# Kernel optimization log

Measured on AMD Instinct MI355X. Metric: run time of the kernel, lower is better.

The kernel has to match this reference:

```python
import jax, jax.numpy as jnp
import numpy as np
from jax import lax

DN = ('NCHW', 'OIHW', 'NCHW')

def conv(x, w, b, stride=1, pad=0):
    y = lax.conv_general_dilated(x, w, (stride, stride), ((pad, pad), (pad, pad)), dimension_numbers=DN)
    return y + b[None, :, None, None]

def conv_transpose(x, w, b):
    # torch ConvTranspose2d(k=4, s=2, p=1): w is (in_ch, out_ch, 4, 4)
    wf = jnp.flip(w, (2, 3)).transpose(1, 0, 2, 3)  # -> (out_ch, in_ch, 4, 4)
    pad = 4 - 1 - 1  # k - 1 - p = 2
    y = lax.conv_general_dilated(x, wf, (1, 1), ((pad, pad), (pad, pad)), lhs_dilation=(2, 2), dimension_numbers=DN)
    return y + b[None, :, None, None]

def setup_inputs() -> dict:
    key = jax.random.key(0)
    ks = jax.random.split(key, 16)
    HID, ZC, K = 256, 64, 512
    def w(k, shape):
        return (jax.random.normal(k, shape, jnp.float32) * 0.02)
    z = lambda n: jnp.zeros((n,), jnp.float32)
    return {
        'x': jax.random.uniform(ks[0], (8, 3, 128, 128), jnp.float32),
        'c1_w': w(ks[1], (HID, 3, 4, 4)), 'c1_b': z(HID),
        'c2_w': w(ks[2], (HID, HID, 4, 4)), 'c2_b': z(HID),
        'r0_w3': w(ks[3], (HID, HID, 3, 3)), 'r0_b3': z(HID),
        'r0_w1': w(ks[4], (HID, HID, 1, 1)), 'r0_b1': z(HID),
        'r1_w3': w(ks[5], (HID, HID, 3, 3)), 'r1_b3': z(HID),
        'r1_w1': w(ks[6], (HID, HID, 1, 1)), 'r1_b1': z(HID),
        'to_z_w': w(ks[7], (ZC, HID, 1, 1)), 'to_z_b': z(ZC),
        'codebook': jax.random.uniform(ks[8], (K, ZC), jnp.float32, -1.0 / K, 1.0 / K),
        'from_z_w': w(ks[9], (HID, ZC, 1, 1)), 'from_z_b': z(HID),
        't1_w': w(ks[10], (HID, HID, 4, 4)), 't1_b': z(HID),
        't2_w': w(ks[11], (HID, 3, 4, 4)), 't2_b': z(3),
    }

def _vqvae(x, c1_w, c1_b, c2_w, c2_b, r0_w3, r0_b3, r0_w1, r0_b1,
           r1_w3, r1_b3, r1_w1, r1_b1, to_z_w, to_z_b, codebook,
           from_z_w, from_z_b, t1_w, t1_b, t2_w, t2_b):
    # ---- Encoder ----
    h = jax.nn.relu(conv(x, c1_w, c1_b, stride=2, pad=1))
    h = jax.nn.relu(conv(h, c2_w, c2_b, stride=2, pad=1))
    for (w3, b3, w1, b1) in ((r0_w3, r0_b3, r0_w1, r0_b1), (r1_w3, r1_b3, r1_w1, r1_b1)):
        r = conv(jax.nn.relu(h), w3, b3, pad=1)
        r = conv(jax.nn.relu(r), w1, b1)
        h = h + r
    z_e = conv(h, to_z_w, to_z_b)  # [B, ZC, H/4, W/4]
    # ---- Vector quantization ----
    B, C, H, W = z_e.shape
    z_flat = z_e.transpose(0, 2, 3, 1).reshape(-1, C)  # [N, C]
    dist = (jnp.sum(z_flat * z_flat, axis=1, keepdims=True)
            - 2.0 * z_flat @ codebook.T
            + jnp.sum(codebook * codebook, axis=1)[None, :])  # [N, K]
    ids = jnp.argmin(dist, axis=1)  # [N]
    e_k_flat = codebook[ids]  # [N, C]
    e_k_st_flat = z_flat + lax.stop_gradient(e_k_flat - z_flat)
    e_k = e_k_flat.reshape(B, H, W, C).transpose(0, 3, 1, 2)
    e_k_st = e_k_st_flat.reshape(B, H, W, C).transpose(0, 3, 1, 2)
    ids = ids.reshape(B, H, W)
    # ---- Decoder ----
    d = jax.nn.relu(conv(e_k_st, from_z_w, from_z_b))
    d = jax.nn.relu(conv_transpose(d, t1_w, t1_b))
    out = jax.nn.sigmoid(conv_transpose(d, t2_w, t2_b))
    return out, z_e, e_k, ids

def reference(x, c1_w, c1_b, c2_w, c2_b, r0_w3, r0_b3, r0_w1, r0_b1,
              r1_w3, r1_b3, r1_w1, r1_b1, to_z_w, to_z_b, codebook,
              from_z_w, from_z_b, t1_w, t1_b, t2_w, t2_b):
    return _vqvae(x, c1_w, c1_b, c2_w, c2_b, r0_w3, r0_b3, r0_w1, r0_b1,
                  r1_w3, r1_b3, r1_w1, r1_b1, to_z_w, to_z_b, codebook,
                  from_z_w, from_z_b, t1_w, t1_b, t2_w, t2_b)
```

## Files before the change

### kernel.cpp

```cpp
#include <hip/hip_runtime.h>
#include <math.h>


typedef unsigned int uint;
typedef unsigned short ushort_t;
using short8 = __attribute__((ext_vector_type(8))) short;
using f32x4  = __attribute__((ext_vector_type(4))) float;

__device__ __attribute__((aligned(16))) ushort_t g_zpad[512];

static __device__ __forceinline__ int rfl(int x) { return __builtin_amdgcn_readfirstlane(x); }
static __device__ __forceinline__ ushort_t f2bf(float f) {
  uint u = __float_as_uint(f);
  return (ushort_t)((u + 0x7fffu + ((u >> 16) & 1u)) >> 16);
}
static __device__ __forceinline__ float bf2f(ushort_t b) {
  return __uint_as_float(((uint)b) << 16);
}
static __device__ __forceinline__ void gload16(const ushort_t* g, void* l) {
  __builtin_amdgcn_global_load_lds(
      (const __attribute__((address_space(1))) void*)g,
      (__attribute__((address_space(3))) void*)l, 16, 0, 0);
}

__global__ __launch_bounds__(256) void k_prep_misc(
    const float* __restrict__ c1w, float* __restrict__ wt_c1,
    const float* __restrict__ tozw, float* __restrict__ wt_toz,
    const float* __restrict__ fromzw, float* __restrict__ wt_fromz,
    const float* __restrict__ cb, float* __restrict__ cnorm,
    const float* __restrict__ t2w, ushort_t* __restrict__ w2pk)
{
  const int b = blockIdx.x, tid = threadIdx.x;
  if (b < 48) {
    int idx = b * 256 + tid;
    int co = idx % 256, i = idx / 256;
    wt_c1[idx] = c1w[co * 48 + i];
  } else if (b < 112) {
    int idx = (b - 48) * 256 + tid;
    int co = idx % 64, i = idx / 64;
    wt_toz[idx] = tozw[co * 256 + i];
  } else if (b < 176) {
    int idx = (b - 112) * 256 + tid;
    int co = idx % 256, i = idx / 256;
    wt_fromz[idx] = fromzw[co * 64 + i];
  } else if (b < 178) {
    int idx = (b - 176) * 256 + tid;
    if (idx < 512) {
      float s = 0.f;
      for (int c = 0; c < 64; ++c) { float v = cb[idx * 64 + c]; s = fmaf(v, v, s); }
      cnorm[idx] = s;
    }
  } else {
    int idx = (b - 178) * 256 + tid;
    int k = idx & 31, co = (idx >> 5) & 15, chunk = (idx >> 9) & 31, par = idx >> 14;
    int tap = chunk >> 3, cg = chunk & 7;
    int a = tap >> 1, bb = tap & 1;
    int ry = par & 1, rx = (par >> 1) & 1;
    int ky = ((ry + 1) & 1) + 2 * a;
    int kx = ((rx + 1) & 1) + 2 * bb;
    int ci = cg * 32 + k;
    float v = (co < 3) ? t2w[((ci * 3 + co) << 4) + ky * 4 + kx] : 0.f;
    w2pk[idx] = f2bf(v);
  }
}

template<int KIND>
__global__ __launch_bounds__(256) void k_prep_enc(
    const float* __restrict__ w, ushort_t* __restrict__ wp)
{
  constexpr int KK = (KIND == 0) ? 16 : (KIND == 1 ? 9 : 1);
  constexpr int KW = (KIND == 0) ? 4  : (KIND == 1 ? 3 : 1);
  constexpr int NT = KK;
  const int tid = threadIdx.x;
  const int wvg = blockIdx.x * 4 + (tid >> 6);
  const int lane = tid & 63;
  const int co = wvg >> 2;
  const int ci = (wvg & 3) * 64 + lane;
  const float* src = w + (size_t)(co * 256 + ci) * KK;
  const int coT = co >> 6, row = co & 63, cg = ci >> 5, k = ci & 31;
  float v[KK];
#pragma unroll
  for (int j = 0; j < KK; ++j) v[j] = src[j];
#pragma unroll
  for (int tap = 0; tap < NT; ++tap) {
    int ky, kx;
    if (KIND == 0)      { ky = tap >> 2; kx = tap & 3; }
    else if (KIND == 1) { ky = tap / 3;  kx = tap - ky * 3; }
    else                { ky = 0; kx = 0; }
    float val = v[ky * KW + kx];
    ushort_t b0 = f2bf(val);
    ushort_t b1 = f2bf(val - bf2f(b0));
    const int chunk = tap * 8 + cg;
    size_t base = ((size_t)(chunk * 4 + coT) << 12) + row * 32 + k;
    wp[base] = b0;
    wp[base + 2048] = b1;
  }
}

template<int KIND>
__global__ __launch_bounds__(256) void k_prep_enc2(
    const float* __restrict__ wa, ushort_t* __restrict__ oa,
    const float* __restrict__ wb2, ushort_t* __restrict__ ob)
{
  constexpr int KK = (KIND == 0) ? 16 : (KIND == 1 ? 9 : 1);
  constexpr int KW = (KIND == 0) ? 4  : (KIND == 1 ? 3 : 1);
  constexpr int NT = KK;
  const float* w = (blockIdx.x < 256) ? wa : wb2;
  ushort_t* wp = (blockIdx.x < 256) ? oa : ob;
  const int bx = blockIdx.x & 255;
  const int tid = threadIdx.x;
  const int wvg = bx * 4 + (tid >> 6);
  const int lane = tid & 63;
  const int co = wvg >> 2;
  const int ci = (wvg & 3) * 64 + lane;
  const float* src = w + (size_t)(co * 256 + ci) * KK;
  const int coT = co >> 6, row = co & 63, cg = ci >> 5, k = ci & 31;
  float v[KK];
#pragma unroll
  for (int j = 0; j < KK; ++j) v[j] = src[j];
#pragma unroll
  for (int tap = 0; tap < NT; ++tap) {
    int ky, kx;
    if (KIND == 0)      { ky = tap >> 2; kx = tap & 3; }
    else if (KIND == 1) { ky = tap / 3;  kx = tap - ky * 3; }
    else                { ky = 0; kx = 0; }
    float val = v[ky * KW + kx];
    ushort_t b0 = f2bf(val);
    ushort_t b1 = f2bf(val - bf2f(b0));
    const int chunk = tap * 8 + cg;
    size_t base = ((size_t)(chunk * 4 + coT) << 12) + row * 32 + k;
    wp[base] = b0;
    wp[base + 2048] = b1;
  }
}

__global__ void k_prep_t1w(const float* __restrict__ w, ushort_t* __restrict__ wb) {
  int idx = blockIdx.x * 256 + threadIdx.x;
  int kk  = idx & 31;
  int co  = (idx >> 5) & 255;
  int c8  = (idx >> 13) & 7;
  int tap = (idx >> 16) & 3;
  int par = idx >> 18;
  int ry = par & 1, rx = (par >> 1) & 1;
  int a = tap >> 1, b = tap & 1;
  int ky = ((ry + 1) & 1) + 2 * a;
  int kx = ((rx + 1) & 1) + 2 * b;
  int ci = c8 * 32 + kk;
  wb[idx] = f2bf(w[((ci * 256 + co) << 4) + ky * 4 + kx]);
}

__global__ __launch_bounds__(256) void k_conv1_split(
    const float* __restrict__ in, ushort_t* __restrict__ o0, ushort_t* __restrict__ o1,
    const float* __restrict__ wT, const float* __restrict__ bias)
{
  __shared__ float s_in[3 * 360];
  const int tid = threadIdx.x;
  const int lane = tid & 63;
  const int wv = rfl(tid >> 6);
  const int px = lane & 7, py = lane >> 3;
  const int tx = blockIdx.x & 7, ty = blockIdx.x >> 3;
  const int X = tx * 8, Y = ty * 8;
  const int cob = blockIdx.y * 64 + wv * 16;
  const int n = blockIdx.z;
  float acc[16];
#pragma unroll
  for (int i = 0; i < 16; ++i) acc[i] = bias[cob + i];
  const float* inN = in + (size_t)n * 3 * 16384;
  for (int e = tid; e < 3 * 360; e += 256) {
    int col2 = e % 20; int t = e / 20; int row = t % 18; int ci = t / 18;
    int pr = col2 / 10, hc = col2 % 10, ixl = 2 * hc + pr;
    int iy = 2 * Y - 1 + row, ix = 2 * X - 1 + ixl;
    float v = 0.f;
    if (ixl < 18 && (unsigned)iy < 128u && (unsigned)ix < 128u)
      v = inN[ci * 16384 + iy * 128 + ix];
    s_in[e] = v;
  }
  __syncthreads();
  const float* wc = wT + cob;
#pragma unroll
  for (int c = 0; c < 3; ++c) {
    const float* base = s_in + c * 360 + py * 40 + px;
#pragma unroll
    for (int ky = 0; ky < 4; ++ky) {
#pragma unroll
      for (int kx = 0; kx < 4; ++kx) {
        float iv = base[ky * 20 + (kx & 1) * 10 + (kx >> 1)];
        const float* w = wc + (size_t)(c * 16 + ky * 4 + kx) * 256;
#pragma unroll
        for (int i = 0; i < 16; ++i) acc[i] = fmaf(iv, w[i], acc[i]);
      }
    }
  }
  const int pxg = n * 4096 + (Y + py) * 64 + (X + px);
  uint p0[8], p1[8];
#pragma unroll
  for (int i = 0; i < 8; ++i) {
    float va = fmaxf(acc[2 * i], 0.f), vb = fmaxf(acc[2 * i + 1], 0.f);
    ushort_t a0 = f2bf(va), b0 = f2bf(vb);
    ushort_t a1 = f2bf(va - bf2f(a0)), b1 = f2bf(vb - bf2f(b0));
    p0[i] = (uint)a0 | ((uint)b0 << 16);
    p1[i] = (uint)a1 | ((uint)b1 << 16);
  }
  ushort_t* d0 = o0 + (size_t)pxg * 256 + cob;
  ushort_t* d1 = o1 + (size_t)pxg * 256 + cob;
  uint4 v0a; v0a.x = p0[0]; v0a.y = p0[1]; v0a.z = p0[2]; v0a.w = p0[3];
  uint4 v0b; v0b.x = p0[4]; v0b.y = p0[5]; v0b.z = p0[6]; v0b.w = p0[7];
  uint4 v1a; v1a.x = p1[0]; v1a.y = p1[1]; v1a.z = p1[2]; v1a.w = p1[3];
  uint4 v1b; v1b.x = p1[4]; v1b.y = p1[5]; v1b.z = p1[6]; v1b.w = p1[7];
  *(uint4*)d0 = v0a; *(uint4*)(d0 + 8) = v0b;
  *(uint4*)d1 = v1a; *(uint4*)(d1 + 8) = v1b;
}

template<int KIND>
__global__ __launch_bounds__(256) void k_enc_mfma_split(
    const ushort_t* __restrict__ x0, const ushort_t* __restrict__ x1,
    const ushort_t* __restrict__ wp, float* __restrict__ part)
{
  __shared__ ushort_t smem[2][12288];
  const int tid = threadIdx.x, lane = tid & 63, wv = tid >> 6;
  const int l15 = lane & 15, q = lane >> 4;
  const int pxT = blockIdx.x, coT = blockIdx.y;
  constexpr int NCH = (KIND == 0) ? 128 : 72;
  const int CH0 = blockIdx.z * (NCH / 2), CH1 = CH0 + NCH / 2;
  f32x4 acc[4][2];
#pragma unroll
  for (int m = 0; m < 4; ++m)
#pragma unroll
    for (int n = 0; n < 2; ++n) acc[m][n] = (f32x4){0.f, 0.f, 0.f, 0.f};

  const int r0 = tid >> 2, kq = tid & 3;
  int bimg[2], bu[2], bvc[2];
#pragma unroll
  for (int r = 0; r < 2; ++r) {
    int bpx = pxT * 128 + r0 + r * 64;
    bimg[r] = bpx >> 10; int bp = bpx & 1023; bu[r] = bp >> 5; bvc[r] = bp & 31;
  }
  const ushort_t* srcB[2][2];
  int ptap = -1;
  auto retap = [&](int tap) {
    ptap = tap;
    int ky, kx;
    if (KIND == 0) { ky = tap >> 2; kx = tap & 3; }
    else           { ky = tap / 3;  kx = tap - ky * 3; }
#pragma unroll
    for (int r = 0; r < 2; ++r) {
      bool v; size_t rowb;
      if (KIND == 0) {
        int iy = 2 * bu[r] - 1 + ky, ix = 2 * bvc[r] - 1 + kx;
        v = ((unsigned)iy < 64u) && ((unsigned)ix < 64u);
        rowb = ((size_t)(bimg[r] * 4096 + iy * 64 + ix)) << 8;
      } else {
        int iy = bu[r] - 1 + ky, ix = bvc[r] - 1 + kx;
        v = ((unsigned)iy < 32u) && ((unsigned)ix < 32u);
        rowb = ((size_t)(bimg[r] * 1024 + iy * 32 + ix)) << 8;
      }
      srcB[r][0] = (v ? (x0 + rowb) : g_zpad) + kq * 8;
      srcB[r][1] = (v ? (x1 + rowb) : g_zpad) + kq * 8;
    }
  };

  const int wvb = wv * 1024;
  auto stage = [&](int chunk, int bi) {
    const int tap = chunk >> 3, cg = chunk & 7;
    if (tap != ptap) retap(tap);
    char* bufb = (char*)smem[bi];
    const ushort_t* ap = wp + ((size_t)(chunk * 4 + coT) << 12) + tid * 8;
    gload16(ap,        bufb + wvb);
    gload16(ap + 2048, bufb + 4096 + wvb);
    const int ko = cg * 32;
    gload16(srcB[0][0] + ko, bufb + 8192 + wvb);
    gload16(srcB[1][0] + ko, bufb + 8192 + 4096 + wvb);
    gload16(srcB[0][1] + ko, bufb + 16384 + wvb);
    gload16(srcB[1][1] + ko, bufb + 16384 + 4096 + wvb);
  };
  auto compute = [&](const ushort_t* buf) {
    const ushort_t* sA = buf;
    const ushort_t* sB = buf + 4096;
    short8 af[4][2], bf[2][2];
#pragma unroll
    for (int m = 0; m < 4; ++m)
#pragma unroll
      for (int pl = 0; pl < 2; ++pl)
        af[m][pl] = *(const short8*)(sA + pl * 2048 + (m * 16 + l15) * 32 + q * 8);
#pragma unroll
    for (int n = 0; n < 2; ++n)
#pragma unroll
      for (int pl = 0; pl < 2; ++pl)
        bf[n][pl] = *(const short8*)(sB + pl * 4096 + (wv * 32 + n * 16 + l15) * 32 + q * 8);
#pragma unroll
    for (int m = 0; m < 4; ++m)
#pragma unroll
      for (int n = 0; n < 2; ++n) {
        acc[m][n] = __builtin_amdgcn_mfma_f32_16x16x32_bf16(af[m][0], bf[n][0], acc[m][n], 0, 0, 0);
        acc[m][n] = __builtin_amdgcn_mfma_f32_16x16x32_bf16(af[m][0], bf[n][1], acc[m][n], 0, 0, 0);
        acc[m][n] = __builtin_amdgcn_mfma_f32_16x16x32_bf16(af[m][1], bf[n][0], acc[m][n], 0, 0, 0);
      }
  };

  stage(CH0, 0);
  __syncthreads();
  int cur = 0;
  for (int c = CH0; c < CH1; ++c) {
    if (c + 1 < CH1) stage(c + 1, cur ^ 1);
    compute(smem[cur]);
    __syncthreads();
    cur ^= 1;
  }

  float* pz = part + ((size_t)blockIdx.z << 21);
#pragma unroll
  for (int m = 0; m < 4; ++m) {
#pragma unroll
    for (int n = 0; n < 2; ++n) {
#pragma unroll
      for (int r = 0; r < 4; ++r) {
        const int co_l = m * 16 + q * 4 + r;
        const int px_l = wv * 32 + n * 16 + l15;
        const int px = pxT * 128 + px_l;
        const int img = px >> 10, pp = px & 1023;
        const size_t ha = ((size_t)(img * 256 + coT * 64 + co_l)) * 1024 + pp;
        pz[ha] = acc[m][n][r];
      }
    }
  }
}

__global__ __launch_bounds__(256) void k_enc_mfma_3x3h(
    const ushort_t* __restrict__ x0, const ushort_t* __restrict__ x1,
    const ushort_t* __restrict__ wp, float* __restrict__ part)
{
  __shared__ ushort_t smem[32768];
  const int tid = threadIdx.x, lane = tid & 63, wv = tid >> 6;
  const int l15 = lane & 15, q = lane >> 4;
  const int pxT = blockIdx.x, coT = blockIdx.y;
  const int CG0 = blockIdx.z * 4;
  const int img = pxT >> 3;
  const int U0 = (pxT & 7) * 4;
  f32x4 acc[2][2];
#pragma unroll
  for (int m = 0; m < 2; ++m)
#pragma unroll
    for (int n = 0; n < 2; ++n) acc[m][n] = (f32x4){0.f, 0.f, 0.f, 0.f};

  const ushort_t* srcp[7];
#pragma unroll
  for (int i = 0; i < 7; ++i) {
    int slot = i * 256 + tid;
    int pl = slot >= 816 ? 1 : 0;
    int rem = slot - pl * 816;
    int rr = rem / 136;
    int c4 = rem - rr * 136;
    int cc = c4 >> 2, kq2 = c4 & 3;
    int iy = U0 - 1 + rr, ix = cc - 1;
    bool valid = (slot < 1632) && ((unsigned)iy < 32u) && ((unsigned)ix < 32u);
    const ushort_t* base = valid
        ? ((pl ? x1 : x0) + (((size_t)(img * 1024 + iy * 32 + ix)) << 8))
        : g_zpad;
    srcp[i] = base + kq2 * 8;
  }
  const int apl = tid >> 7;
  const int aus = apl * 2048 + (coT & 1) * 1024 + (tid & 127) * 8;
  const int coTq = coT >> 1;
  const int wvb = wv * 1024;
  char* bufb = (char*)smem;

  for (int cg = CG0; cg < CG0 + 4; ++cg) {
#pragma unroll
    for (int tap = 0; tap < 9; ++tap) {
      const int chunk = tap * 8 + cg;
      gload16(wp + ((size_t)(chunk * 4 + coTq) << 12) + aus, bufb + tap * 4096 + wvb);
    }
    const int ko = cg * 32;
#pragma unroll
    for (int i = 0; i < 7; ++i)
      gload16(srcp[i] + ko, bufb + 36864 + i * 4096 + wvb);
    __syncthreads();
    const ushort_t* Ab = smem;
    const ushort_t* Hb = smem + 18432;
#pragma unroll 3
    for (int tap = 0; tap < 9; ++tap) {
      const int ky = tap / 3, kx = tap - ky * 3;
      short8 af[2][2], bf[2][2];
#pragma unroll
      for (int m = 0; m < 2; ++m)
#pragma unroll
        for (int pl = 0; pl < 2; ++pl)
          af[m][pl] = *(const short8*)(Ab + tap * 2048 + pl * 1024 + (m * 16 + l15) * 32 + q * 8);
      const int r = wv + ky;
#pragma unroll
      for (int n = 0; n < 2; ++n)
#pragma unroll
        for (int pl = 0; pl < 2; ++pl)
          bf[n][pl] = *(const short8*)(Hb + pl * 6528 + r * 1088 + (n * 16 + l15 + kx) * 32 + q * 8);
#pragma unroll
      for (int m = 0; m < 2; ++m)
#pragma unroll
        for (int n = 0; n < 2; ++n) {
          acc[m][n] = __builtin_amdgcn_mfma_f32_16x16x32_bf16(af[m][0], bf[n][0], acc[m][n], 0, 0, 0);
          acc[m][n] = __builtin_amdgcn_mfma_f32_16x16x32_bf16(af[m][0], bf[n][1], acc[m][n], 0, 0, 0);
          acc[m][n] = __builtin_amdgcn_mfma_f32_16x16x32_bf16(af[m][1], bf[n][0], acc[m][n], 0, 0, 0);
        }
    }
    __syncthreads();
  }

  float* pz = part + ((size_t)blockIdx.z << 21);
#pragma unroll
  for (int m = 0; m < 2; ++m) {
#pragma unroll
    for (int n = 0; n < 2; ++n) {
#pragma unroll
      for (int r = 0; r < 4; ++r) {
        const int co_l = m * 16 + q * 4 + r;
        const int px_l = wv * 32 + n * 16 + l15;
        const int px = pxT * 128 + px_l;
        const int imgp = px >> 10, pp = px & 1023;
        const size_t ha = ((size_t)(imgp * 256 + coT * 32 + co_l)) * 1024 + pp;
        pz[ha] = acc[m][n][r];
      }
    }
  }
}

template<bool WH>
__global__ __launch_bounds__(256) void k_enc_epi(
    const float* __restrict__ part, float* __restrict__ h32,
    ushort_t* __restrict__ s0, ushort_t* __restrict__ s1,
    const float* __restrict__ bias)
{
  const int px = blockIdx.x * 256 + threadIdx.x;
  const int co0 = blockIdx.y * 16;
  const int img = px >> 10, pp = px & 1023;
  const float* part1 = part + (1u << 21);
  uint p0[8], p1[8];
#pragma unroll
  for (int i = 0; i < 8; ++i) {
    size_t ha = ((size_t)(img * 256 + co0 + 2 * i)) * 1024 + pp;
    size_t hb = ha + 1024;
    float va = part[ha] + part1[ha] + bias[co0 + 2 * i];
    float vb = part[hb] + part1[hb] + bias[co0 + 2 * i + 1];
    float sa, sb;
    if (WH) {
      va = fmaxf(va, 0.f); vb = fmaxf(vb, 0.f);
      h32[ha] = va; h32[hb] = vb; sa = va; sb = vb;
    } else { sa = fmaxf(va, 0.f); sb = fmaxf(vb, 0.f); }
    ushort_t a0 = f2bf(sa), b0 = f2bf(sb);
    p0[i] = (uint)a0 | ((uint)b0 << 16);
    p1[i] = (uint)f2bf(sa - bf2f(a0)) | ((uint)f2bf(sb - bf2f(b0)) << 16);
  }
  ushort_t* d0 = s0 + (size_t)px * 256 + co0;
  ushort_t* d1 = s1 + (size_t)px * 256 + co0;
  uint4 v0a; v0a.x = p0[0]; v0a.y = p0[1]; v0a.z = p0[2]; v0a.w = p0[3];
  uint4 v0b; v0b.x = p0[4]; v0b.y = p0[5]; v0b.z = p0[6]; v0b.w = p0[7];
  uint4 v1a; v1a.x = p1[0]; v1a.y = p1[1]; v1a.z = p1[2]; v1a.w = p1[3];
  uint4 v1b; v1b.x = p1[4]; v1b.y = p1[5]; v1b.z = p1[6]; v1b.w = p1[7];
  *(uint4*)d0 = v0a; *(uint4*)(d0 + 8) = v0b;
  *(uint4*)d1 = v1a; *(uint4*)(d1 + 8) = v1b;
}

template<bool WS>
__global__ __launch_bounds__(256) void k_enc_mfma(
    const ushort_t* __restrict__ x0, const ushort_t* __restrict__ x1,
    const ushort_t* __restrict__ wp, const float* __restrict__ bias,
    float* __restrict__ h32, ushort_t* __restrict__ sp0, ushort_t* __restrict__ sp1)
{
  __shared__ ushort_t smem[24576];
  const int tid = threadIdx.x, lane = tid & 63, wv = tid >> 6;
  const int l15 = lane & 15, q = lane >> 4;
  const int pxT = blockIdx.x, coT = blockIdx.y;
  f32x4 acc[4][2];
#pragma unroll
  for (int m = 0; m < 4; ++m)
#pragma unroll
    for (int n = 0; n < 2; ++n) acc[m][n] = (f32x4){0.f, 0.f, 0.f, 0.f};

  const int r0 = tid >> 2, kq = tid & 3;
  const ushort_t* srcB[2][2];
#pragma unroll
  for (int r = 0; r < 2; ++r) {
    size_t rowb = ((size_t)(pxT * 128 + r0 + r * 64)) << 8;
    srcB[r][0] = x0 + rowb + kq * 8;
    srcB[r][1] = x1 + rowb + kq * 8;
  }
  const int wvb = wv * 1024;
  auto stage = [&](int c, int bi) {
    char* bufb = (char*)(smem + bi * 12288);
    const ushort_t* ap = wp + ((size_t)(c * 4 + coT) << 12) + tid * 8;
    gload16(ap,        bufb + wvb);
    gload16(ap + 2048, bufb + 4096 + wvb);
    const int ko = c * 32;
    gload16(srcB[0][0] + ko, bufb + 8192 + wvb);
    gload16(srcB[1][0] + ko, bufb + 8192 + 4096 + wvb);
    gload16(srcB[0][1] + ko, bufb + 16384 + wvb);
    gload16(srcB[1][1] + ko, bufb + 16384 + 4096 + wvb);
  };
  auto compute = [&](const ushort_t* buf) {
    const ushort_t* sA = buf;
    const ushort_t* sB = buf + 4096;
    short8 af[4][2], bf[2][2];
#pragma unroll
    for (int m = 0; m < 4; ++m)
#pragma unroll
      for (int pl = 0; pl < 2; ++pl)
        af[m][pl] = *(const short8*)(sA + pl * 2048 + (m * 16 + l15) * 32 + q * 8);
#pragma unroll
    for (int n = 0; n < 2; ++n)
#pragma unroll
      for (int pl = 0; pl < 2; ++pl)
        bf[n][pl] = *(const short8*)(sB + pl * 4096 + (wv * 32 + n * 16 + l15) * 32 + q * 8);
#pragma unroll
    for (int m = 0; m < 4; ++m)
#pragma unroll
      for (int n = 0; n < 2; ++n) {
        acc[m][n] = __builtin_amdgcn_mfma_f32_16x16x32_bf16(af[m][0], bf[n][0], acc[m][n], 0, 0, 0);
        acc[m][n] = __builtin_amdgcn_mfma_f32_16x16x32_bf16(af[m][0], bf[n][1], acc[m][n], 0, 0, 0);
        acc[m][n] = __builtin_amdgcn_mfma_f32_16x16x32_bf16(af[m][1], bf[n][0], acc[m][n], 0, 0, 0);
      }
  };

  stage(0, 0);
  __syncthreads();
  int cur = 0;
  for (int c = 0; c < 8; ++c) {
    if (c + 1 < 8) stage(c + 1, cur ^ 1);
    compute(smem + cur * 12288);
    __syncthreads();
    cur ^= 1;
  }

#pragma unroll
  for (int m = 0; m < 4; ++m) {
#pragma unroll
    for (int n = 0; n < 2; ++n) {
#pragma unroll
      for (int r = 0; r < 4; ++r) {
        const int co_l = m * 16 + q * 4 + r;
        const int px_l = wv * 32 + n * 16 + l15;
        float v = acc[m][n][r] + bias[coT * 64 + co_l];
        const int px = pxT * 128 + px_l;
        const int img = px >> 10, pp = px & 1023;
        const size_t ha = ((size_t)(img * 256 + coT * 64 + co_l)) * 1024 + pp;
        v += h32[ha];
        h32[ha] = v;
        if (WS) {
          float sv = fmaxf(v, 0.f);
          ushort_t b0 = f2bf(sv);
          smem[px_l * 72 + co_l] = b0;
          smem[9216 + px_l * 72 + co_l] = f2bf(sv - bf2f(b0));
        }
      }
    }
  }
  if (WS) {
    __syncthreads();
#pragma unroll
    for (int i = 0; i < 8; ++i) {
      int idx = tid + 256 * i;
      int pl = idx >> 10, w2 = idx & 1023, pxl = w2 >> 3, g = w2 & 7;
      uint4 vv = *(const uint4*)(smem + pl * 9216 + pxl * 72 + g * 8);
      ushort_t* dst = (pl ? sp1 : sp0) + ((size_t)(pxT * 128 + pxl)) * 256 + coT * 64 + g * 8;
      *(uint4*)dst = vv;
    }
  }
}

__global__ __launch_bounds__(256) void k_conv1x1(
    const float* __restrict__ in, float* __restrict__ out,
    const float* __restrict__ wT, const float* __restrict__ bias,
    int CI, int CO, int P)
{
  const int p = blockIdx.x * 256 + threadIdx.x;
  const int cob = blockIdx.y * 16;
  const int n = blockIdx.z;
  const float* inN = in + (size_t)n * CI * P + p;
  float acc[16];
#pragma unroll
  for (int i = 0; i < 16; ++i) acc[i] = bias[cob + i];
  const float* wr = wT + cob;
#pragma unroll 4
  for (int ci = 0; ci < CI; ++ci) {
    float iv = inN[(size_t)ci * P];
    const float* w = wr + (size_t)ci * CO;
#pragma unroll
    for (int i = 0; i < 16; ++i) acc[i] = fmaf(iv, w[i], acc[i]);
  }
  float* outN = out + (size_t)n * CO * P + p;
#pragma unroll
  for (int i = 0; i < 16; ++i) outN[(size_t)(cob + i) * P] = acc[i];
}

__global__ __launch_bounds__(256) void k_vq_part(
    const float* __restrict__ z_e, const float* __restrict__ cb,
    const float* __restrict__ cnorm, float* __restrict__ pbest, int* __restrict__ pbid)
{
  int g = blockIdx.x * 256 + threadIdx.x;
  int chunk = blockIdx.y;
  int img = g >> 10, p = g & 1023;
  const float* zp = z_e + (size_t)img * 64 * 1024 + p;
  float z[64];
#pragma unroll
  for (int c = 0; c < 64; ++c) z[c] = zp[(size_t)c * 1024];
  float best = 3.4e38f; int bid = chunk << 5;
  const int j0 = chunk << 5;
  for (int j = j0; j < j0 + 32; ++j) {
    const float* cj = cb + j * 64;
    float m = 0.f;
#pragma unroll
    for (int c = 0; c < 64; ++c) m = fmaf(z[c], cj[c], m);
    float d = fmaf(-2.f, m, cnorm[j]);
    if (d < best) { best = d; bid = j; }
  }
  pbest[chunk * 8192 + g] = best;
  pbid[chunk * 8192 + g] = bid;
}

__global__ __launch_bounds__(256) void k_vq_reduce(
    const float* __restrict__ pbest, const int* __restrict__ pbid,
    const float* __restrict__ cb, float* __restrict__ ids_f, float* __restrict__ ek)
{
  int g = blockIdx.x * 256 + threadIdx.x;
  float best = 3.4e38f; int bid = 0;
#pragma unroll
  for (int ch = 0; ch < 16; ++ch) {
    float d = pbest[ch * 8192 + g];
    int b = pbid[ch * 8192 + g];
    if (d < best) { best = d; bid = b; }
  }
  ids_f[g] = (float)bid;
  int img = g >> 10, p = g & 1023;
  const float* cbid = cb + bid * 64;
  float* ekp = ek + (size_t)img * 64 * 1024 + p;
#pragma unroll
  for (int c = 0; c < 64; ++c) ekp[(size_t)c * 1024] = cbid[c];
}

__global__ __launch_bounds__(256) void k_from_z(
    const float* __restrict__ ek, ushort_t* __restrict__ nhwc,
    const float* __restrict__ wT, const float* __restrict__ bias)
{
  const int p = blockIdx.x * 256 + threadIdx.x;
  const int co0 = blockIdx.y * 16;
  const int n = blockIdx.z;
  const float* inN = ek + (size_t)n * 64 * 1024 + p;
  float acc[16];
#pragma unroll
  for (int i = 0; i < 16; ++i) acc[i] = bias[co0 + i];
#pragma unroll 4
  for (int ci = 0; ci < 64; ++ci) {
    float iv = inN[(size_t)ci * 1024];
    const float* w = wT + (size_t)ci * 256 + co0;
#pragma unroll
    for (int i = 0; i < 16; ++i) acc[i] = fmaf(iv, w[i], acc[i]);
  }
  uint pk[8];
#pragma unroll
  for (int i = 0; i < 8; ++i) {
    ushort_t lo = f2bf(fmaxf(acc[2 * i], 0.f));
    ushort_t hi = f2bf(fmaxf(acc[2 * i + 1], 0.f));
    pk[i] = (uint)lo | ((uint)hi << 16);
  }
  ushort_t* op = nhwc + (((size_t)n * 1024 + p) * 256 + co0);
  uint4 v0; v0.x = pk[0]; v0.y = pk[1]; v0.z = pk[2]; v0.w = pk[3];
  uint4 v1; v1.x = pk[4]; v1.y = pk[5]; v1.z = pk[6]; v1.w = pk[7];
  *(uint4*)(op) = v0;
  *(uint4*)(op + 8) = v1;
}

__global__ __launch_bounds__(256) void k_mfma_t1(
    const ushort_t* __restrict__ nhwc, const ushort_t* __restrict__ wb,
    const float* __restrict__ bias, ushort_t* __restrict__ t1o)
{
  __shared__ ushort_t smem[2][8192];
  const int tid = threadIdx.x;
  const int lane = tid & 63;
  const int wv = tid >> 6;
  const int wm = wv & 1, wn = wv >> 1;
  const int l15 = lane & 15, q = lane >> 4;
  const int pxT = blockIdx.x, coT = blockIdx.y, par = blockIdx.z;
  const int ry = par & 1, rx = (par >> 1) & 1;
  const int pxbase = pxT * 128;
  const int img = pxbase >> 10;
  f32x4 acc[4][4];
#pragma unroll
  for (int i = 0; i < 4; ++i)
#pragma unroll
    for (int j = 0; j < 4; ++j) acc[i][j] = (f32x4){0.f, 0.f, 0.f, 0.f};

  const int srow = tid >> 2, kg = tid & 3;
  int bu2[2], bv2[2];
#pragma unroll
  for (int r = 0; r < 2; ++r) {
    int px = pxbase + srow + r * 64;
    bu2[r] = (px >> 5) & 31; bv2[r] = px & 31;
  }
  const ushort_t* nb[2];
  int ptap = -1;
  auto retap = [&](int tap) {
    ptap = tap;
    int ta = tap >> 1, tb = tap & 1;
#pragma unroll
    for (int r = 0; r < 2; ++r) {
      int iy = bu2[r] + ry - ta, ix = bv2[r] + rx - tb;
      bool v = ((unsigned)iy < 32u) && ((unsigned)ix < 32u);
      nb[r] = (v ? (nhwc + (((size_t)(img * 1024 + iy * 32 + ix)) << 8)) : g_zpad) + kg * 8;
    }
  };
  const int wvb = wv * 1024;
  auto stage = [&](int c, int bi) {
    const int tap = c >> 3, c8 = c & 7;
    if (tap != ptap) retap(tap);
    char* bufb = (char*)smem[bi];
    const ushort_t* Abase = wb + ((size_t)((par * 4 + tap) * 8 + c8) << 13) + coT * 4096 + tid * 8;
    gload16(Abase,        bufb + wvb);
    gload16(Abase + 2048, bufb + 4096 + wvb);
    const int ko = c8 * 32;
    gload16(nb[0] + ko, bufb + 8192 + wvb);
    gload16(nb[1] + ko, bufb + 8192 + 4096 + wvb);
  };
  auto compute = [&](const ushort_t* buf) {
    const ushort_t* sA = buf;
    const ushort_t* sB = buf + 4096;
    short8 af[4], bfr[4];
#pragma unroll
    for (int i = 0; i < 4; ++i)
      af[i] = *(const short8*)(sA + (wm * 64 + i * 16 + l15) * 32 + q * 8);
#pragma unroll
    for (int j = 0; j < 4; ++j)
      bfr[j] = *(const short8*)(sB + (wn * 64 + j * 16 + l15) * 32 + q * 8);
#pragma unroll
    for (int i = 0; i < 4; ++i)
#pragma unroll
      for (int j = 0; j < 4; ++j)
        acc[i][j] = __builtin_amdgcn_mfma_f32_16x16x32_bf16(af[i], bfr[j], acc[i][j], 0, 0, 0);
  };

  stage(0, 0);
  __syncthreads();
  int cur = 0;
  for (int c = 0; c < 32; ++c) {
    if (c + 1 < 32) stage(c + 1, cur ^ 1);
    compute(smem[cur]);
    __syncthreads();
    cur ^= 1;
  }

#pragma unroll
  for (int i = 0; i < 4; ++i) {
    int co = coT * 128 + wm * 64 + i * 16 + q * 4;
#pragma unroll
    for (int j = 0; j < 4; ++j) {
      int px = pxbase + wn * 64 + j * 16 + l15;
      int u = (px >> 5) & 31, vv = px & 31;
      int oy = 2 * u + ry, ox = 2 * vv + rx;
      ushort_t e0 = f2bf(fmaxf(acc[i][j][0] + bias[co + 0], 0.f));
      ushort_t e1 = f2bf(fmaxf(acc[i][j][1] + bias[co + 1], 0.f));
      ushort_t e2 = f2bf(fmaxf(acc[i][j][2] + bias[co + 2], 0.f));
      ushort_t e3 = f2bf(fmaxf(acc[i][j][3] + bias[co + 3], 0.f));
      uint2 pk; pk.x = (uint)e0 | ((uint)e1 << 16); pk.y = (uint)e2 | ((uint)e3 << 16);
      *(uint2*)(t1o + ((size_t)(img * 4096 + oy * 64 + ox) * 256 + co)) = pk;
    }
  }
}

__global__ __launch_bounds__(256) void k_mfma_t2(
    const ushort_t* __restrict__ t1o, const ushort_t* __restrict__ wb,
    const float* __restrict__ bias, float* __restrict__ out)
{
  __shared__ ushort_t sA2[256 * 32];
  __shared__ ushort_t sB2[16 * 32];
  const int tid = threadIdx.x, lane = tid & 63, wv = tid >> 6;
  const int l15 = lane & 15, q = lane >> 4;
  const int pxb = blockIdx.x * 256;
  const int par = blockIdx.y;
  const int ry = par & 1, rx = (par >> 1) & 1;
  f32x4 acc[4];
#pragma unroll
  for (int m = 0; m < 4; ++m) acc[m] = (f32x4){0.f, 0.f, 0.f, 0.f};
  const int kg = tid & 3;
  const int ssw = ((tid >> 2) & 7) << 3;
  size_t rb[4]; bool rv[4];
  for (int chunk = 0; chunk < 32; ++chunk) {
    const int tap = chunk >> 3, cg = chunk & 7;
    const int a = tap >> 1, b = tap & 1;
    if ((chunk & 7) == 0) {
#pragma unroll
      for (int i = 0; i < 4; ++i) {
        int row = (tid >> 2) + 64 * i;
        int px = pxb + row;
        int img = px >> 12, p = px & 4095, u = p >> 6, v = p & 63;
        int iy = u + ry - a, ix = v + rx - b;
        rv[i] = ((unsigned)iy < 64u) && ((unsigned)ix < 64u);
        rb[i] = ((size_t)(img * 4096 + iy * 64 + ix)) << 8;
      }
    }
    uint4 av[4];
#pragma unroll
    for (int i = 0; i < 4; ++i) {
      if (rv[i]) av[i] = *(const uint4*)(t1o + rb[i] + cg * 32 + kg * 8);
      else { av[i].x = 0; av[i].y = 0; av[i].z = 0; av[i].w = 0; }
    }
    uint4 bv;
    if (tid < 64) bv = *(const uint4*)(wb + ((size_t)(par * 32 + chunk)) * 512 + tid * 8);
    __syncthreads();
#pragma unroll
    for (int i = 0; i < 4; ++i)
      *(uint4*)(sA2 + (((((tid >> 2) + 64 * i) * 32) + kg * 8) ^ ssw)) = av[i];
    if (tid < 64) *(uint4*)(sB2 + ((tid * 8) ^ ssw)) = bv;
    __syncthreads();
    short8 bf = *(const short8*)(sB2 + ((l15 * 32 + q * 8) ^ ((l15 & 7) << 3)));
#pragma unroll
    for (int m = 0; m < 4; ++m) {
      const int row = wv * 64 + m * 16 + l15;
      short8 af = *(const short8*)(sA2 + ((row * 32 + q * 8) ^ ((row & 7) << 3)));
      acc[m] = __builtin_amdgcn_mfma_f32_16x16x32_bf16(af, bf, acc[m], 0, 0, 0);
    }
    __syncthreads();
  }
  const int co = l15;
  if (co < 3) {
    float bco = bias[co];
#pragma unroll
    for (int m = 0; m < 4; ++m) {
#pragma unroll
      for (int r = 0; r < 4; ++r) {
        int px = pxb + wv * 64 + m * 16 + q * 4 + r;
        int img = px >> 12, p = px & 4095, u = p >> 6, v = p & 63;
        size_t addr = ((size_t)(img * 3 + co)) * 16384 + (2 * u + ry) * 128 + (2 * v + rx);
        out[addr] = 1.f / (1.f + expf(-(acc[m][r] + bco)));
      }
    }
  }
}

extern "C" void kernel_launch(void* const* d_in, const int* in_sizes, int n_in,
                              void* d_out, int out_size, void* d_ws, size_t ws_size,
                              hipStream_t stream) {
  (void)in_sizes; (void)n_in; (void)out_size; (void)ws_size;
  const float* x      = (const float*)d_in[0];
  const float* c1_w   = (const float*)d_in[1];
  const float* c1_b   = (const float*)d_in[2];
  const float* c2_w   = (const float*)d_in[3];
  const float* c2_b   = (const float*)d_in[4];
  const float* r0_w3  = (const float*)d_in[5];
  const float* r0_b3  = (const float*)d_in[6];
  const float* r0_w1  = (const float*)d_in[7];
  const float* r0_b1  = (const float*)d_in[8];
  const float* r1_w3  = (const float*)d_in[9];
  const float* r1_b3  = (const float*)d_in[10];
  const float* r1_w1  = (const float*)d_in[11];
  const float* r1_b1  = (const float*)d_in[12];
  const float* to_z_w = (const float*)d_in[13];
  const float* to_z_b = (const float*)d_in[14];
  const float* cb     = (const float*)d_in[15];
  const float* from_z_w = (const float*)d_in[16];
  const float* from_z_b = (const float*)d_in[17];
  const float* t1_w   = (const float*)d_in[18];
  const float* t1_b   = (const float*)d_in[19];
  const float* t2_w   = (const float*)d_in[20];
  const float* t2_b   = (const float*)d_in[21];

  float* wsf = (float*)d_ws;
  ushort_t* xs1p0 = (ushort_t*)(wsf + 0);
  ushort_t* xs1p1 = (ushort_t*)(wsf + 4194304);
  float*    cp0   = wsf + 8388608;
  float*    h32   = wsf + 8388608;
  float*    qp0   = wsf + 4194304;
  ushort_t* sE0   = (ushort_t*)(wsf + 0);
  ushort_t* sE1   = (ushort_t*)(wsf + 1048576);
  ushort_t* sF0   = (ushort_t*)(wsf + 2097152);
  ushort_t* sF1   = (ushort_t*)(wsf + 3145728);
  float*    pbest = wsf + 0;
  int*      pbid  = (int*)(wsf + 131072);
  ushort_t* t1out = (ushort_t*)(wsf + 2097152);
  ushort_t* decn  = (ushort_t*)(wsf + 6291456);
  ushort_t* wp_c2   = (ushort_t*)(wsf + 12582912);
  ushort_t* wp_r0w3 = (ushort_t*)(wsf + 13631488);
  ushort_t* wp_r1w3 = (ushort_t*)(wsf + 14221312);
  ushort_t* wp_r0w1 = (ushort_t*)(wsf + 14811136);
  ushort_t* wp_r1w1 = (ushort_t*)(wsf + 14876672);
  float*    wt_c1   = wsf + 14942208;
  float*    wt_toz  = wsf + 14954496;
  float*    wt_fromz= wsf + 14970880;
  ushort_t* t1wb    = (ushort_t*)(wsf + 14987264);
  ushort_t* w2pk    = (ushort_t*)(wsf + 15511552);
  float*    cnorm   = wsf + 15544320;

  float* out_img = (float*)d_out;
  float* z_e_out = out_img + 393216;
  float* e_k_out = z_e_out + 524288;
  float* ids_out = e_k_out + 524288;

  k_prep_misc<<<434, 256, 0, stream>>>(c1_w, wt_c1, to_z_w, wt_toz,
                                       from_z_w, wt_fromz, cb, cnorm, t2_w, w2pk);
  k_prep_enc<0><<<256, 256, 0, stream>>>(c2_w, wp_c2);
  k_prep_enc2<1><<<512, 256, 0, stream>>>(r0_w3, wp_r0w3, r1_w3, wp_r1w3);
  k_prep_enc2<2><<<512, 256, 0, stream>>>(r0_w1, wp_r0w1, r1_w1, wp_r1w1);
  k_prep_t1w<<<4096, 256, 0, stream>>>(t1_w, t1wb);

  k_conv1_split<<<dim3(64, 4, 8), 256, 0, stream>>>(x, xs1p0, xs1p1, wt_c1, c1_b);
  k_enc_mfma_split<0><<<dim3(64, 4, 2), 256, 0, stream>>>(xs1p0, xs1p1, wp_c2, cp0);
  k_enc_epi<true><<<dim3(32, 16), 256, 0, stream>>>(cp0, h32, sE0, sE1, c2_b);
  k_enc_mfma_3x3h<<<dim3(64, 8, 2), 256, 0, stream>>>(sE0, sE1, wp_r0w3, qp0);
  k_enc_epi<false><<<dim3(32, 16), 256, 0, stream>>>(qp0, nullptr, sE0, sE1, r0_b3);
  k_enc_mfma<true ><<<dim3(64, 4), 256, 0, stream>>>(
      sE0, sE1, wp_r0w1, r0_b1, h32, sF0, sF1);
  k_enc_mfma_3x3h<<<dim3(64, 8, 2), 256, 0, stream>>>(sF0, sF1, wp_r1w3, qp0);
  k_enc_epi<false><<<dim3(32, 16), 256, 0, stream>>>(qp0, nullptr, sE0, sE1, r1_b3);
  k_enc_mfma<false><<<dim3(64, 4), 256, 0, stream>>>(
      sE0, sE1, wp_r1w1, r1_b1, h32, nullptr, nullptr);
  k_conv1x1<<<dim3(4, 4, 8), 256, 0, stream>>>(h32, z_e_out, wt_toz, to_z_b, 256, 64, 1024);

  k_vq_part<<<dim3(32, 16), 256, 0, stream>>>(z_e_out, cb, cnorm, pbest, pbid);
  k_vq_reduce<<<32, 256, 0, stream>>>(pbest, pbid, cb, ids_out, e_k_out);

  k_from_z<<<dim3(4, 16, 8), 256, 0, stream>>>(e_k_out, decn, wt_fromz, from_z_b);
  k_mfma_t1<<<dim3(64, 2, 4), 256, 0, stream>>>(decn, t1wb, t1_b, t1out);
  k_mfma_t2<<<dim3(128, 4), 256, 0, stream>>>(t1out, w2pk, t2_b, out_img);
}
```

Before: 409.4 us.

## Share halo input tile across taps in t1 and double-buffer t2 with async LDS loads

The t1 transposed-conv kernel now stages a halo tile of input rows (6x34 pixels) once per channel chunk and reuses it for all four taps, loading all four tap weight slices at once. This replaces 32 per-tap stages with 8 larger ones, cutting redundant input loads and half the barriers, but it drops double buffering so loads no longer overlap compute. The t2 kernel switches from register-staged swizzled stores to double-buffered global_load_lds prefetching with zero-pad pointers. That removes the XOR swizzle and may add LDS bank conflicts.

```diff
diff --git a/kernel.cpp b/kernel.cpp
--- a/kernel.cpp
+++ b/kernel.cpp
@@ -670,7 +670,7 @@
     const ushort_t* __restrict__ nhwc, const ushort_t* __restrict__ wb,
     const float* __restrict__ bias, ushort_t* __restrict__ t1o)
 {
-  __shared__ ushort_t smem[2][8192];
+  __shared__ ushort_t smem[24576];
   const int tid = threadIdx.x;
   const int lane = tid & 63;
   const int wv = tid >> 6;
@@ -680,68 +680,66 @@
   const int ry = par & 1, rx = (par >> 1) & 1;
   const int pxbase = pxT * 128;
   const int img = pxbase >> 10;
+  const int U0 = (pxT & 7) * 4;
   f32x4 acc[4][4];
 #pragma unroll
   for (int i = 0; i < 4; ++i)
 #pragma unroll
     for (int j = 0; j < 4; ++j) acc[i][j] = (f32x4){0.f, 0.f, 0.f, 0.f};
 
-  const int srow = tid >> 2, kg = tid & 3;
-  int bu2[2], bv2[2];
-#pragma unroll
-  for (int r = 0; r < 2; ++r) {
-    int px = pxbase + srow + r * 64;
-    bu2[r] = (px >> 5) & 31; bv2[r] = px & 31;
-  }
-  const ushort_t* nb[2];
-  int ptap = -1;
-  auto retap = [&](int tap) {
-    ptap = tap;
-    int ta = tap >> 1, tb = tap & 1;
-#pragma unroll
-    for (int r = 0; r < 2; ++r) {
-      int iy = bu2[r] + ry - ta, ix = bv2[r] + rx - tb;
-      bool v = ((unsigned)iy < 32u) && ((unsigned)ix < 32u);
-      nb[r] = (v ? (nhwc + (((size_t)(img * 1024 + iy * 32 + ix)) << 8)) : g_zpad) + kg * 8;
-    }
-  };
+  const ushort_t* srcp[4];
+#pragma unroll
+  for (int i = 0; i < 4; ++i) {
+    int slot = i * 256 + tid;
+    int rr = slot / 136;
+    int c4 = slot - rr * 136;
+    int cc = c4 >> 2, kq2 = c4 & 3;
+    int iy = U0 - 1 + rr, ix = cc - 1;
+    bool valid = (slot < 816) && ((unsigned)iy < 32u) && ((unsigned)ix < 32u);
+    const ushort_t* base = valid
+        ? (nhwc + (((size_t)(img * 1024 + iy * 32 + ix)) << 8))
+        : g_zpad;
+    srcp[i] = base + kq2 * 8;
+  }
   const int wvb = wv * 1024;
-  auto stage = [&](int c, int bi) {
-    const int tap = c >> 3, c8 = c & 7;
-    if (tap != ptap) retap(tap);
-    char* bufb = (char*)smem[bi];
-    const ushort_t* Abase = wb + ((size_t)((par * 4 + tap) * 8 + c8) << 13) + coT * 4096 + tid * 8;
-    gload16(Abase,        bufb + wvb);
-    gload16(Abase + 2048, bufb + 4096 + wvb);
+  char* bufb = (char*)smem;
+
+  for (int c8 = 0; c8 < 8; ++c8) {
+#pragma unroll
+    for (int tap = 0; tap < 4; ++tap) {
+      const ushort_t* Ab = wb + ((size_t)((par * 4 + tap) * 8 + c8) << 13)
+                           + coT * 4096 + tid * 8;
+      gload16(Ab,        bufb + tap * 8192 + wvb);
+      gload16(Ab + 2048, bufb + tap * 8192 + 4096 + wvb);
+    }
     const int ko = c8 * 32;
-    gload16(nb[0] + ko, bufb + 8192 + wvb);
-    gload16(nb[1] + ko, bufb + 8192 + 4096 + wvb);
-  };
-  auto compute = [&](const ushort_t* buf) {
-    const ushort_t* sA = buf;
-    const ushort_t* sB = buf + 4096;
-    short8 af[4], bfr[4];
 #pragma unroll
     for (int i = 0; i < 4; ++i)
-      af[i] = *(const short8*)(sA + (wm * 64 + i * 16 + l15) * 32 + q * 8);
-#pragma unroll
-    for (int j = 0; j < 4; ++j)
-      bfr[j] = *(const short8*)(sB + (wn * 64 + j * 16 + l15) * 32 + q * 8);
-#pragma unroll
-    for (int i = 0; i < 4; ++i)
-#pragma unroll
-      for (int j = 0; j < 4; ++j)
-        acc[i][j] = __builtin_amdgcn_mfma_f32_16x16x32_bf16(af[i], bfr[j], acc[i][j], 0, 0, 0);
-  };
-
-  stage(0, 0);
-  __syncthreads();
-  int cur = 0;
-  for (int c = 0; c < 32; ++c) {
-    if (c + 1 < 32) stage(c + 1, cur ^ 1);
-    compute(smem[cur]);
+      gload16(srcp[i] + ko, bufb + 32768 + i * 4096 + wvb);
     __syncthreads();
-    cur ^= 1;
+    const ushort_t* A = smem;
+    const ushort_t* H = smem + 16384;
+#pragma unroll
+    for (int tap = 0; tap < 4; ++tap) {
+      const int a = tap >> 1, b = tap & 1;
+      const int dr = ry + 1 - a, dc = rx + 1 - b;
+      short8 af[4], bfr[4];
+#pragma unroll
+      for (int i = 0; i < 4; ++i)
+        af[i] = *(const short8*)(A + tap * 4096 + (wm * 64 + i * 16 + l15) * 32 + q * 8);
+#pragma unroll
+      for (int j = 0; j < 4; ++j) {
+        const int row = wn * 64 + j * 16 + l15;
+        const int rr = (row >> 5) + dr, cc = (row & 31) + dc;
+        bfr[j] = *(const short8*)(H + rr * 1088 + cc * 32 + q * 8);
+      }
+#pragma unroll
+      for (int i = 0; i < 4; ++i)
+#pragma unroll
+        for (int j = 0; j < 4; ++j)
+          acc[i][j] = __builtin_amdgcn_mfma_f32_16x16x32_bf16(af[i], bfr[j], acc[i][j], 0, 0, 0);
+    }
+    __syncthreads();
   }
 
 #pragma unroll
@@ -766,8 +764,7 @@
     const ushort_t* __restrict__ t1o, const ushort_t* __restrict__ wb,
     const float* __restrict__ bias, float* __restrict__ out)
 {
-  __shared__ ushort_t sA2[256 * 32];
-  __shared__ ushort_t sB2[16 * 32];
+  __shared__ ushort_t smem[2][8704];
   const int tid = threadIdx.x, lane = tid & 63, wv = tid >> 6;
   const int l15 = lane & 15, q = lane >> 4;
   const int pxb = blockIdx.x * 256;
@@ -777,45 +774,56 @@
 #pragma unroll
   for (int m = 0; m < 4; ++m) acc[m] = (f32x4){0.f, 0.f, 0.f, 0.f};
   const int kg = tid & 3;
-  const int ssw = ((tid >> 2) & 7) << 3;
-  size_t rb[4]; bool rv[4];
-  for (int chunk = 0; chunk < 32; ++chunk) {
-    const int tap = chunk >> 3, cg = chunk & 7;
+  const ushort_t* srcA[4];
+  int ptap = -1;
+  auto retap = [&](int tap) {
+    ptap = tap;
     const int a = tap >> 1, b = tap & 1;
-    if ((chunk & 7) == 0) {
-#pragma unroll
-      for (int i = 0; i < 4; ++i) {
-        int row = (tid >> 2) + 64 * i;
-        int px = pxb + row;
-        int img = px >> 12, p = px & 4095, u = p >> 6, v = p & 63;
-        int iy = u + ry - a, ix = v + rx - b;
-        rv[i] = ((unsigned)iy < 64u) && ((unsigned)ix < 64u);
-        rb[i] = ((size_t)(img * 4096 + iy * 64 + ix)) << 8;
-      }
-    }
-    uint4 av[4];
 #pragma unroll
     for (int i = 0; i < 4; ++i) {
-      if (rv[i]) av[i] = *(const uint4*)(t1o + rb[i] + cg * 32 + kg * 8);
-      else { av[i].x = 0; av[i].y = 0; av[i].z = 0; av[i].w = 0; }
-    }
-    uint4 bv;
-    if (tid < 64) bv = *(const uint4*)(wb + ((size_t)(par * 32 + chunk)) * 512 + tid * 8);
-    __syncthreads();
+      int row = (tid >> 2) + 64 * i;
+      int px = pxb + row;
+      int img = px >> 12, p = px & 4095, u = p >> 6, v = p & 63;
+      int iy = u + ry - a, ix = v + rx - b;
+      bool valid = ((unsigned)iy < 64u) && ((unsigned)ix < 64u);
+      srcA[i] = (valid ? (t1o + (((size_t)(img * 4096 + iy * 64 + ix)) << 8)) : g_zpad)
+                + kg * 8;
+    }
+  };
+  const int wvb = wv * 1024;
+  auto stage = [&](int c, int bi) {
+    const int tap = c >> 3, cg = c & 7;
+    if (tap != ptap) retap(tap);
+    char* bufb = (char*)smem[bi];
+    const int ko = cg * 32;
 #pragma unroll
     for (int i = 0; i < 4; ++i)
-      *(uint4*)(sA2 + (((((tid >> 2) + 64 * i) * 32) + kg * 8) ^ ssw)) = av[i];
-    if (tid < 64) *(uint4*)(sB2 + ((tid * 8) ^ ssw)) = bv;
-    __syncthreads();
-    short8 bf = *(const short8*)(sB2 + ((l15 * 32 + q * 8) ^ ((l15 & 7) << 3)));
+      gload16(srcA[i] + ko, bufb + i * 4096 + wvb);
+    if (tid < 64)
+      gload16(wb + ((size_t)(par * 32 + c)) * 512 + tid * 8, bufb + 16384);
+  };
+  auto compute = [&](const ushort_t* buf) {
+    const ushort_t* sA = buf;
+    const ushort_t* sB = buf + 8192;
+    short8 bf = *(const short8*)(sB + l15 * 32 + q * 8);
 #pragma unroll
     for (int m = 0; m < 4; ++m) {
       const int row = wv * 64 + m * 16 + l15;
-      short8 af = *(const short8*)(sA2 + ((row * 32 + q * 8) ^ ((row & 7) << 3)));
+      short8 af = *(const short8*)(sA + row * 32 + q * 8);
       acc[m] = __builtin_amdgcn_mfma_f32_16x16x32_bf16(af, bf, acc[m], 0, 0, 0);
     }
+  };
+
+  stage(0, 0);
+  __syncthreads();
+  int cur = 0;
+  for (int c = 0; c < 32; ++c) {
+    if (c + 1 < 32) stage(c + 1, cur ^ 1);
+    compute(smem[cur]);
     __syncthreads();
-  }
+    cur ^= 1;
+  }
+
   const int co = l15;
   if (co < 3) {
     float bco = bias[co];
```

New measurement: 403.3 us. No clear change (-1.5%).
